# Optimization experiments

Hardware: AMD Instinct MI355X
Metric: run time of the kernel (lower is better)

Reference implementation:

```python
import jax, jax.numpy as jnp
import numpy as np

MARGIN = 1.0


def setup_inputs() -> dict:
    key = jax.random.key(0)
    k1, k2, k3 = jax.random.split(key, 3)
    B, D, C = 16384, 256, 2000
    pred_embedding = jax.random.normal(k1, (B, D), dtype=jnp.float32)
    batch_label = jax.random.randint(k2, (B,), 0, C, dtype=jnp.int64)
    train_classes = jnp.arange(C, dtype=jnp.int64)
    train_sig = jax.random.normal(k3, (D, C), dtype=jnp.float32)
    return {
        "pred_embedding": pred_embedding,
        "batch_label": batch_label,
        "train_classes": train_classes,
        "train_sig": train_sig,
    }


def reference(pred_embedding, batch_label, train_classes, train_sig):
    # scores[j, k] = <pred_embedding[j], train_sig[:, train_classes[k]]>
    # Single GEMM replaces the per-pair dot-product loops.
    sig_cols = train_sig[:, train_classes]            # [D, C]
    scores = jnp.einsum("bd,dc->bc", pred_embedding, sig_cols)  # [B, C]
    # ground-truth class score per row: <XW_j, train_sig[:, y_j]>
    gt = jnp.einsum("bd,db->b", pred_embedding, train_sig[:, batch_label])  # [B]
    # exclude the class equal to the row label
    mask = (train_classes[None, :] != batch_label[:, None])  # [B, C] bool
    hinge = jnp.maximum(MARGIN + scores - gt[:, None], 0.0)
    loss = jnp.sum(jnp.where(mask, hinge, 0.0))
    return loss
```

## Files before the change

### kernel.cpp

```cpp
#include <hip/hip_runtime.h>

#define B_SZ 16384
#define D_SZ 256
#define C_SZ 2000
#define C_PAD 2048
#define MARGIN_F 1.0f
#define NBLK 1024

typedef __bf16 bf16x8 __attribute__((ext_vector_type(8)));
typedef float floatx16 __attribute__((ext_vector_type(16)));

__device__ inline void gld_lds16(const void* g, void* l) {
  __builtin_amdgcn_global_load_lds(
      (const __attribute__((address_space(1))) void*)g,
      (__attribute__((address_space(3))) void*)l, 16, 0, 0);
}


__global__ __launch_bounds__(256) void prep_kernel(
    const float* __restrict__ pred, const float* __restrict__ sig,
    const int* __restrict__ label, __bf16* __restrict__ predf,
    __bf16* __restrict__ sigf, float* __restrict__ gt,
    float* __restrict__ corr) {
  int bid = (int)blockIdx.x;
  int tid = threadIdx.x;
  if (bid < 512) {
    __shared__ float ldsP[32][257];
#pragma unroll
    for (int it = 0; it < 8; it++) {
      int idx = it * 1024 + tid * 4;
      int r = idx >> 8, c = idx & 255;
      float4 v = *(const float4*)(pred + (size_t)(bid * 32 + r) * D_SZ + c);
      ldsP[r][c] = v.x; ldsP[r][c + 1] = v.y;
      ldsP[r][c + 2] = v.z; ldsP[r][c + 3] = v.w;
    }
    __syncthreads();
#pragma unroll
    for (int it = 0; it < 4; it++) {
      int ch = it * 256 + tid;
      int lane = ch & 63, ks = ch >> 6;
      int r = lane & 31, kb = ks * 16 + (lane >> 5) * 8;
      bf16x8 o;
#pragma unroll
      for (int j = 0; j < 8; j++) o[j] = (__bf16)ldsP[r][kb + j];
      *(bf16x8*)(predf + ((size_t)(bid * 16 + ks) * 64 + lane) * 8) = o;
    }
    int lane = tid & 63, w = tid >> 6;
    for (int rr = 0; rr < 8; rr++) {
      int r = w * 8 + rr;
      int row = bid * 32 + r;
      int lbl = label[row];
      float sf = 0.f, sb = 0.f;
#pragma unroll
      for (int i = 0; i < 4; i++) {
        float p = ldsP[r][lane * 4 + i];
        float s = sig[(size_t)(lane * 4 + i) * C_SZ + lbl];
        sf += p * s;
        sb += (float)(__bf16)p * (float)(__bf16)s;
      }
#pragma unroll
      for (int off = 32; off > 0; off >>= 1) {
        sf += __shfl_down(sf, off, 64);
        sb += __shfl_down(sb, off, 64);
      }
      if (lane == 0) {
        gt[row] = sf;
        corr[row] = fmaxf(MARGIN_F + sb - sf, 0.f);
      }
    }
  } else {
    int ct = bid - 512;
#pragma unroll
    for (int it = 0; it < 4; it++) {
      int ch = it * 256 + tid;
      int lane = ch & 63, ks = ch >> 6;
      int col = ct * 32 + (lane & 31);
      int kb = ks * 16 + (lane >> 5) * 8;
      bf16x8 o;
      if (col < C_SZ) {
#pragma unroll
        for (int j = 0; j < 8; j++) o[j] = (__bf16)sig[(size_t)(kb + j) * C_SZ + col];
      } else {
#pragma unroll
        for (int j = 0; j < 8; j++) o[j] = (__bf16)0.f;
      }
      *(bf16x8*)(sigf + ((size_t)(ct * 16 + ks) * 64 + lane) * 8) = o;
    }
  }
}

__global__ __launch_bounds__(256, 2) void mfma_fused_kernel(
    const __bf16* __restrict__ predf, const __bf16* __restrict__ sigf,
    const float* __restrict__ gt, float* __restrict__ partial) {
  __shared__ __bf16 Bs[4096 * 8];
  __shared__ float red[4];
  int tid = threadIdx.x;
  int lane = tid & 63;
  int w = tid >> 6;
  int kh = lane >> 5, lm = lane & 31;
  int bid = (int)blockIdx.x;
  int i = bid >> 3;
  int rsb = (bid & 7) * 8 + (i & 7);
  int cg = i >> 3;

#pragma unroll
  for (int s = 0; s < 16; s++) {
    int q0 = s * 256 + w * 64;
    gld_lds16(sigf + ((size_t)cg * 4096 + q0 + lane) * 8, (void*)(Bs + (size_t)q0 * 8));
  }

  bf16x8 afr[2][16];
#pragma unroll
  for (int rt = 0; rt < 2; rt++)
#pragma unroll
    for (int ks = 0; ks < 16; ks++)
      afr[rt][ks] = *(const bf16x8*)(predf +
          (((size_t)(rsb * 8 + w * 2 + rt) * 16 + ks) * 64 + lane) * 8);

  float mgv[2][16];
#pragma unroll
  for (int rt = 0; rt < 2; rt++)
#pragma unroll
    for (int reg = 0; reg < 16; reg++) {
      int row = rsb * 256 + w * 64 + rt * 32 + (reg & 3) + 8 * (reg >> 2) + 4 * kh;
      mgv[rt][reg] = MARGIN_F - gt[row];
    }
  __syncthreads();

  float sum = 0.f;
  for (int ct = 0; ct < 4; ct++) {
    floatx16 acc0 = {}, acc1 = {};
#pragma unroll
    for (int ks = 0; ks < 16; ks++) {
      bf16x8 bfr = *(const bf16x8*)(Bs + (size_t)((ct * 16 + ks) * 64 + lane) * 8);
      acc0 = __builtin_amdgcn_mfma_f32_32x32x16_bf16(afr[0][ks], bfr, acc0, 0, 0, 0);
      acc1 = __builtin_amdgcn_mfma_f32_32x32x16_bf16(afr[1][ks], bfr, acc1, 0, 0, 0);
    }
    int col = cg * 128 + ct * 32 + lm;
    float keep = (col < C_SZ) ? 1.f : 0.f;
#pragma unroll
    for (int reg = 0; reg < 16; reg++) {
      sum += keep * fmaxf(acc0[reg] + mgv[0][reg], 0.f);
      sum += keep * fmaxf(acc1[reg] + mgv[1][reg], 0.f);
    }
  }
#pragma unroll
  for (int off = 32; off > 0; off >>= 1) sum += __shfl_down(sum, off, 64);
  if (lane == 0) red[w] = sum;
  __syncthreads();
  if (tid == 0) partial[bid] = red[0] + red[1] + red[2] + red[3];
}

__global__ __launch_bounds__(256) void reduce_kernel(
    const float* __restrict__ partial, const float* __restrict__ corr,
    float* __restrict__ out) {
  int tid = threadIdx.x;
  float s = 0.f;
  for (int i = tid; i < NBLK; i += 256) s += partial[i];
  for (int i = tid * 4; i < B_SZ; i += 1024) {
    float4 c = *(const float4*)(corr + i);
    s -= c.x + c.y + c.z + c.w;
  }
#pragma unroll
  for (int off = 32; off > 0; off >>= 1) s += __shfl_down(s, off, 64);
  __shared__ float red[4];
  if ((tid & 63) == 0) red[tid >> 6] = s;
  __syncthreads();
  if (tid == 0) out[0] = red[0] + red[1] + red[2] + red[3];
}

extern "C" void kernel_launch(void* const* d_in, const int* in_sizes, int n_in,
                              void* d_out, int out_size, void* d_ws, size_t ws_size,
                              hipStream_t stream) {
  const float* pred  = (const float*)d_in[0];
  const int*   label = (const int*)d_in[1];
  const float* sig   = (const float*)d_in[3];
  float* out = (float*)d_out;

  float*  gt      = (float*)d_ws;
  float*  corr    = (float*)((char*)d_ws + (64 << 10));
  float*  partial = (float*)((char*)d_ws + (128 << 10));
  __bf16* predf   = (__bf16*)((char*)d_ws + (192 << 10));
  __bf16* sigf    = (__bf16*)((char*)d_ws + (192 << 10) + (8 << 20));

  prep_kernel<<<576, 256, 0, stream>>>(pred, sig, label, predf, sigf, gt, corr);
  mfma_fused_kernel<<<NBLK, 256, 0, stream>>>(predf, sigf, gt, partial);
  reduce_kernel<<<1, 256, 0, stream>>>(partial, corr, out);
}
```

Before: 111.7 us.

## Split sig conversion, compute gt in bf16, fold final reduce into GEMM kernel

Moves the sig-to-bf16 packing into its own small kernel so prep can read the label column from the packed bf16 buffer. The ground-truth score is now computed in bf16 so it matches the GEMM diagonal, which removes the correction array. The separate reduce kernel is replaced by a last-block-done atomic counter inside the MFMA kernel, which subtracts the constant B*margin for the label column. This trades one launch for another, still three kernels in total. It also adds a serial dependency between the sig and prep stages and an atomic/fence tail in the main kernel.

```diff
diff --git a/kernel.cpp b/kernel.cpp
--- a/kernel.cpp
+++ b/kernel.cpp
@@ -8,6 +8,7 @@
 #define NBLK 1024
 
 typedef __bf16 bf16x8 __attribute__((ext_vector_type(8)));
+typedef __bf16 bf16x4 __attribute__((ext_vector_type(4)));
 typedef float floatx16 __attribute__((ext_vector_type(16)));
 
 __device__ inline void gld_lds16(const void* g, void* l) {
@@ -17,83 +18,84 @@
 }
 
 
+__global__ __launch_bounds__(256) void sigf_kernel(
+    const float* __restrict__ sig, __bf16* __restrict__ sigf,
+    unsigned int* __restrict__ cnt) {
+  if (blockIdx.x == 0 && threadIdx.x == 0) *cnt = 0u;
+  int ct = (int)blockIdx.x;
+#pragma unroll
+  for (int it = 0; it < 4; it++) {
+    int ch = it * 256 + threadIdx.x;
+    int lane = ch & 63, ks = ch >> 6;
+    int col = ct * 32 + (lane & 31);
+    int kb = ks * 16 + (lane >> 5) * 8;
+    bf16x8 o;
+    if (col < C_SZ) {
+#pragma unroll
+      for (int j = 0; j < 8; j++) o[j] = (__bf16)sig[(size_t)(kb + j) * C_SZ + col];
+    } else {
+#pragma unroll
+      for (int j = 0; j < 8; j++) o[j] = (__bf16)0.f;
+    }
+    *(bf16x8*)(sigf + ((size_t)(ct * 16 + ks) * 64 + lane) * 8) = o;
+  }
+}
+
 __global__ __launch_bounds__(256) void prep_kernel(
-    const float* __restrict__ pred, const float* __restrict__ sig,
+    const float* __restrict__ pred, const __bf16* __restrict__ sigf,
     const int* __restrict__ label, __bf16* __restrict__ predf,
-    __bf16* __restrict__ sigf, float* __restrict__ gt,
-    float* __restrict__ corr) {
+    float* __restrict__ gt) {
+  __shared__ float ldsP[32][257];
   int bid = (int)blockIdx.x;
   int tid = threadIdx.x;
-  if (bid < 512) {
-    __shared__ float ldsP[32][257];
 #pragma unroll
-    for (int it = 0; it < 8; it++) {
-      int idx = it * 1024 + tid * 4;
-      int r = idx >> 8, c = idx & 255;
-      float4 v = *(const float4*)(pred + (size_t)(bid * 32 + r) * D_SZ + c);
-      ldsP[r][c] = v.x; ldsP[r][c + 1] = v.y;
-      ldsP[r][c + 2] = v.z; ldsP[r][c + 3] = v.w;
-    }
-    __syncthreads();
+  for (int it = 0; it < 8; it++) {
+    int idx = it * 1024 + tid * 4;
+    int r = idx >> 8, c = idx & 255;
+    float4 v = *(const float4*)(pred + (size_t)(bid * 32 + r) * D_SZ + c);
+    ldsP[r][c] = v.x; ldsP[r][c + 1] = v.y;
+    ldsP[r][c + 2] = v.z; ldsP[r][c + 3] = v.w;
+  }
+  __syncthreads();
 #pragma unroll
-    for (int it = 0; it < 4; it++) {
-      int ch = it * 256 + tid;
-      int lane = ch & 63, ks = ch >> 6;
-      int r = lane & 31, kb = ks * 16 + (lane >> 5) * 8;
-      bf16x8 o;
+  for (int it = 0; it < 4; it++) {
+    int ch = it * 256 + tid;
+    int lane = ch & 63, ks = ch >> 6;
+    int r = lane & 31, kb = ks * 16 + (lane >> 5) * 8;
+    bf16x8 o;
 #pragma unroll
-      for (int j = 0; j < 8; j++) o[j] = (__bf16)ldsP[r][kb + j];
-      *(bf16x8*)(predf + ((size_t)(bid * 16 + ks) * 64 + lane) * 8) = o;
-    }
-    int lane = tid & 63, w = tid >> 6;
-    for (int rr = 0; rr < 8; rr++) {
-      int r = w * 8 + rr;
-      int row = bid * 32 + r;
-      int lbl = label[row];
-      float sf = 0.f, sb = 0.f;
+    for (int j = 0; j < 8; j++) o[j] = (__bf16)ldsP[r][kb + j];
+    *(bf16x8*)(predf + ((size_t)(bid * 16 + ks) * 64 + lane) * 8) = o;
+  }
+  int lane = tid & 63, w = tid >> 6;
+  for (int rr = 0; rr < 8; rr++) {
+    int r = w * 8 + rr;
+    int row = bid * 32 + r;
+    int lbl = label[row];
+    int tile = lbl >> 5, l5 = lbl & 31;
+    int k0 = lane * 4;
+    int ks = k0 >> 4;
+    int kh = (k0 >> 3) & 1;
+    int j0 = k0 & 7;
+    bf16x4 sb = *(const bf16x4*)(sigf +
+        (((size_t)(tile * 16 + ks) * 64) + kh * 32 + l5) * 8 + j0);
+    float s = 0.f;
 #pragma unroll
-      for (int i = 0; i < 4; i++) {
-        float p = ldsP[r][lane * 4 + i];
-        float s = sig[(size_t)(lane * 4 + i) * C_SZ + lbl];
-        sf += p * s;
-        sb += (float)(__bf16)p * (float)(__bf16)s;
-      }
+    for (int i = 0; i < 4; i++)
+      s += (float)(__bf16)ldsP[r][k0 + i] * (float)sb[i];
 #pragma unroll
-      for (int off = 32; off > 0; off >>= 1) {
-        sf += __shfl_down(sf, off, 64);
-        sb += __shfl_down(sb, off, 64);
-      }
-      if (lane == 0) {
-        gt[row] = sf;
-        corr[row] = fmaxf(MARGIN_F + sb - sf, 0.f);
-      }
-    }
-  } else {
-    int ct = bid - 512;
-#pragma unroll
-    for (int it = 0; it < 4; it++) {
-      int ch = it * 256 + tid;
-      int lane = ch & 63, ks = ch >> 6;
-      int col = ct * 32 + (lane & 31);
-      int kb = ks * 16 + (lane >> 5) * 8;
-      bf16x8 o;
-      if (col < C_SZ) {
-#pragma unroll
-        for (int j = 0; j < 8; j++) o[j] = (__bf16)sig[(size_t)(kb + j) * C_SZ + col];
-      } else {
-#pragma unroll
-        for (int j = 0; j < 8; j++) o[j] = (__bf16)0.f;
-      }
-      *(bf16x8*)(sigf + ((size_t)(ct * 16 + ks) * 64 + lane) * 8) = o;
-    }
+    for (int off = 32; off > 0; off >>= 1) s += __shfl_down(s, off, 64);
+    if (lane == 0) gt[row] = s;
   }
 }
 
 __global__ __launch_bounds__(256, 2) void mfma_fused_kernel(
     const __bf16* __restrict__ predf, const __bf16* __restrict__ sigf,
-    const float* __restrict__ gt, float* __restrict__ partial) {
+    const float* __restrict__ gt, float* __restrict__ partial,
+    unsigned int* __restrict__ cnt, float* __restrict__ out) {
   __shared__ __bf16 Bs[4096 * 8];
   __shared__ float red[4];
+  __shared__ float lastFlag;
   int tid = threadIdx.x;
   int lane = tid & 63;
   int w = tid >> 6;
@@ -148,25 +150,23 @@
   for (int off = 32; off > 0; off >>= 1) sum += __shfl_down(sum, off, 64);
   if (lane == 0) red[w] = sum;
   __syncthreads();
-  if (tid == 0) partial[bid] = red[0] + red[1] + red[2] + red[3];
-}
-
-__global__ __launch_bounds__(256) void reduce_kernel(
-    const float* __restrict__ partial, const float* __restrict__ corr,
-    float* __restrict__ out) {
-  int tid = threadIdx.x;
-  float s = 0.f;
-  for (int i = tid; i < NBLK; i += 256) s += partial[i];
-  for (int i = tid * 4; i < B_SZ; i += 1024) {
-    float4 c = *(const float4*)(corr + i);
-    s -= c.x + c.y + c.z + c.w;
+  if (tid == 0) {
+    partial[bid] = red[0] + red[1] + red[2] + red[3];
+    __threadfence();
+    unsigned int old = atomicAdd(cnt, 1u);
+    lastFlag = (old == NBLK - 1) ? 1.f : 0.f;
   }
+  __syncthreads();
+  if (lastFlag != 0.f) {
+    float s = (tid == 0) ? -(float)B_SZ * MARGIN_F : 0.f;
+    for (int p = tid; p < NBLK; p += 256)
+      s += atomicAdd(&partial[p], 0.f);
 #pragma unroll
-  for (int off = 32; off > 0; off >>= 1) s += __shfl_down(s, off, 64);
-  __shared__ float red[4];
-  if ((tid & 63) == 0) red[tid >> 6] = s;
-  __syncthreads();
-  if (tid == 0) out[0] = red[0] + red[1] + red[2] + red[3];
+    for (int off = 32; off > 0; off >>= 1) s += __shfl_down(s, off, 64);
+    if (lane == 0) red[w] = s;
+    __syncthreads();
+    if (tid == 0) out[0] = red[0] + red[1] + red[2] + red[3];
+  }
 }
 
 extern "C" void kernel_launch(void* const* d_in, const int* in_sizes, int n_in,
@@ -177,13 +177,13 @@
   const float* sig   = (const float*)d_in[3];
   float* out = (float*)d_out;
 
-  float*  gt      = (float*)d_ws;
-  float*  corr    = (float*)((char*)d_ws + (64 << 10));
-  float*  partial = (float*)((char*)d_ws + (128 << 10));
-  __bf16* predf   = (__bf16*)((char*)d_ws + (192 << 10));
-  __bf16* sigf    = (__bf16*)((char*)d_ws + (192 << 10) + (8 << 20));
+  float*        gt      = (float*)d_ws;
+  float*        partial = (float*)((char*)d_ws + (64 << 10));
+  unsigned int* cnt     = (unsigned int*)((char*)d_ws + (68 << 10));
+  __bf16*       predf   = (__bf16*)((char*)d_ws + (128 << 10));
+  __bf16*       sigf    = (__bf16*)((char*)d_ws + (128 << 10) + (8 << 20));
 
-  prep_kernel<<<576, 256, 0, stream>>>(pred, sig, label, predf, sigf, gt, corr);
-  mfma_fused_kernel<<<NBLK, 256, 0, stream>>>(predf, sigf, gt, partial);
-  reduce_kernel<<<1, 256, 0, stream>>>(partial, corr, out);
+  sigf_kernel<<<64, 256, 0, stream>>>(sig, sigf, cnt);
+  prep_kernel<<<512, 256, 0, stream>>>(pred, sigf, label, predf, gt);
+  mfma_fused_kernel<<<NBLK, 256, 0, stream>>>(predf, sigf, gt, partial, cnt, out);
 }
```

After: 114.2 us. 1.02x slower.

## Switch GEMM operands from bf16 to fp8 MFMA and drop diagonal correction pass

Applied to the files above, without the earlier changes.

Quantizes the prediction and signature matrices to fp8 instead of bf16 and uses the fp8 32x32x16 MFMA. This halves operand bytes and LDS footprint and doubles matrix throughput. The ground-truth score is now computed from fp8-rounded values, so the diagonal hinge term equals exactly the margin and is subtracted as a constant instead of through a per-row correction array. The cost is much lower precision in the loss sum, and the result now depends on fp8 rounding matching between the GEMM and the scalar path.

```diff
diff --git a/kernel.cpp b/kernel.cpp
--- a/kernel.cpp
+++ b/kernel.cpp
@@ -7,7 +7,6 @@
 #define MARGIN_F 1.0f
 #define NBLK 1024
 
-typedef __bf16 bf16x8 __attribute__((ext_vector_type(8)));
 typedef float floatx16 __attribute__((ext_vector_type(16)));
 
 __device__ inline void gld_lds16(const void* g, void* l) {
@@ -17,22 +16,31 @@
 }
 
 
+__device__ inline int2 pack8_fp8(const float* v) {
+  int lo = __builtin_amdgcn_cvt_pk_fp8_f32(v[0], v[1], 0, false);
+  lo = __builtin_amdgcn_cvt_pk_fp8_f32(v[2], v[3], lo, true);
+  int hi = __builtin_amdgcn_cvt_pk_fp8_f32(v[4], v[5], 0, false);
+  hi = __builtin_amdgcn_cvt_pk_fp8_f32(v[6], v[7], hi, true);
+  return make_int2(lo, hi);
+}
+__device__ inline float rt_fp8(float x) {
+  int p = __builtin_amdgcn_cvt_pk_fp8_f32(x, x, 0, false);
+  return __builtin_amdgcn_cvt_f32_fp8(p, 0);
+}
+
 __global__ __launch_bounds__(256) void prep_kernel(
     const float* __restrict__ pred, const float* __restrict__ sig,
-    const int* __restrict__ label, __bf16* __restrict__ predf,
-    __bf16* __restrict__ sigf, float* __restrict__ gt,
-    float* __restrict__ corr) {
+    const int* __restrict__ label, char* __restrict__ predq,
+    char* __restrict__ sigq, float* __restrict__ gt) {
   int bid = (int)blockIdx.x;
   int tid = threadIdx.x;
   if (bid < 512) {
-    __shared__ float ldsP[32][257];
+    __shared__ float ldsP[32][260];
 #pragma unroll
     for (int it = 0; it < 8; it++) {
       int idx = it * 1024 + tid * 4;
       int r = idx >> 8, c = idx & 255;
-      float4 v = *(const float4*)(pred + (size_t)(bid * 32 + r) * D_SZ + c);
-      ldsP[r][c] = v.x; ldsP[r][c + 1] = v.y;
-      ldsP[r][c + 2] = v.z; ldsP[r][c + 3] = v.w;
+      *(float4*)&ldsP[r][c] = *(const float4*)(pred + (size_t)(bid * 32 + r) * D_SZ + c);
     }
     __syncthreads();
 #pragma unroll
@@ -40,33 +48,24 @@
       int ch = it * 256 + tid;
       int lane = ch & 63, ks = ch >> 6;
       int r = lane & 31, kb = ks * 16 + (lane >> 5) * 8;
-      bf16x8 o;
+      float v[8];
 #pragma unroll
-      for (int j = 0; j < 8; j++) o[j] = (__bf16)ldsP[r][kb + j];
-      *(bf16x8*)(predf + ((size_t)(bid * 16 + ks) * 64 + lane) * 8) = o;
+      for (int j = 0; j < 8; j++) v[j] = ldsP[r][kb + j];
+      *(int2*)(predq + ((size_t)(bid * 16 + ks) * 64 + lane) * 8) = pack8_fp8(v);
     }
     int lane = tid & 63, w = tid >> 6;
     for (int rr = 0; rr < 8; rr++) {
       int r = w * 8 + rr;
       int row = bid * 32 + r;
       int lbl = label[row];
-      float sf = 0.f, sb = 0.f;
+      float s = 0.f;
 #pragma unroll
-      for (int i = 0; i < 4; i++) {
-        float p = ldsP[r][lane * 4 + i];
-        float s = sig[(size_t)(lane * 4 + i) * C_SZ + lbl];
-        sf += p * s;
-        sb += (float)(__bf16)p * (float)(__bf16)s;
-      }
+      for (int i = 0; i < 4; i++)
+        s += rt_fp8(ldsP[r][lane * 4 + i]) *
+             rt_fp8(sig[(size_t)(lane * 4 + i) * C_SZ + lbl]);
 #pragma unroll
-      for (int off = 32; off > 0; off >>= 1) {
-        sf += __shfl_down(sf, off, 64);
-        sb += __shfl_down(sb, off, 64);
-      }
-      if (lane == 0) {
-        gt[row] = sf;
-        corr[row] = fmaxf(MARGIN_F + sb - sf, 0.f);
-      }
+      for (int off = 32; off > 0; off >>= 1) s += __shfl_down(s, off, 64);
+      if (lane == 0) gt[row] = s;
     }
   } else {
     int ct = bid - 512;
@@ -76,23 +75,19 @@
       int lane = ch & 63, ks = ch >> 6;
       int col = ct * 32 + (lane & 31);
       int kb = ks * 16 + (lane >> 5) * 8;
-      bf16x8 o;
-      if (col < C_SZ) {
+      float v[8];
 #pragma unroll
-        for (int j = 0; j < 8; j++) o[j] = (__bf16)sig[(size_t)(kb + j) * C_SZ + col];
-      } else {
-#pragma unroll
-        for (int j = 0; j < 8; j++) o[j] = (__bf16)0.f;
-      }
-      *(bf16x8*)(sigf + ((size_t)(ct * 16 + ks) * 64 + lane) * 8) = o;
+      for (int j = 0; j < 8; j++)
+        v[j] = (col < C_SZ) ? sig[(size_t)(kb + j) * C_SZ + col] : 0.f;
+      *(int2*)(sigq + ((size_t)(ct * 16 + ks) * 64 + lane) * 8) = pack8_fp8(v);
     }
   }
 }
 
-__global__ __launch_bounds__(256, 2) void mfma_fused_kernel(
-    const __bf16* __restrict__ predf, const __bf16* __restrict__ sigf,
+__global__ __launch_bounds__(256) void mfma_fused_kernel(
+    const char* __restrict__ predq, const char* __restrict__ sigq,
     const float* __restrict__ gt, float* __restrict__ partial) {
-  __shared__ __bf16 Bs[4096 * 8];
+  __shared__ char Bs[4096 * 8];
   __shared__ float red[4];
   int tid = threadIdx.x;
   int lane = tid & 63;
@@ -104,17 +99,17 @@
   int cg = i >> 3;
 
 #pragma unroll
-  for (int s = 0; s < 16; s++) {
+  for (int s = 0; s < 8; s++) {
     int q0 = s * 256 + w * 64;
-    gld_lds16(sigf + ((size_t)cg * 4096 + q0 + lane) * 8, (void*)(Bs + (size_t)q0 * 8));
+    gld_lds16(sigq + ((size_t)cg * 2048 + q0 + lane) * 16, (void*)(Bs + (size_t)q0 * 16));
   }
 
-  bf16x8 afr[2][16];
+  long afr[2][16];
 #pragma unroll
   for (int rt = 0; rt < 2; rt++)
 #pragma unroll
     for (int ks = 0; ks < 16; ks++)
-      afr[rt][ks] = *(const bf16x8*)(predf +
+      afr[rt][ks] = *(const long*)(predq +
           (((size_t)(rsb * 8 + w * 2 + rt) * 16 + ks) * 64 + lane) * 8);
 
   float mgv[2][16];
@@ -128,13 +123,14 @@
   __syncthreads();
 
   float sum = 0.f;
+#pragma unroll
   for (int ct = 0; ct < 4; ct++) {
     floatx16 acc0 = {}, acc1 = {};
 #pragma unroll
     for (int ks = 0; ks < 16; ks++) {
-      bf16x8 bfr = *(const bf16x8*)(Bs + (size_t)((ct * 16 + ks) * 64 + lane) * 8);
-      acc0 = __builtin_amdgcn_mfma_f32_32x32x16_bf16(afr[0][ks], bfr, acc0, 0, 0, 0);
-      acc1 = __builtin_amdgcn_mfma_f32_32x32x16_bf16(afr[1][ks], bfr, acc1, 0, 0, 0);
+      long b = *(const long*)(Bs + (size_t)((ct * 16 + ks) * 64 + lane) * 8);
+      acc0 = __builtin_amdgcn_mfma_f32_32x32x16_fp8_fp8(afr[0][ks], b, acc0, 0, 0, 0);
+      acc1 = __builtin_amdgcn_mfma_f32_32x32x16_fp8_fp8(afr[1][ks], b, acc1, 0, 0, 0);
     }
     int col = cg * 128 + ct * 32 + lm;
     float keep = (col < C_SZ) ? 1.f : 0.f;
@@ -152,21 +148,19 @@
 }
 
 __global__ __launch_bounds__(256) void reduce_kernel(
-    const float* __restrict__ partial, const float* __restrict__ corr,
-    float* __restrict__ out) {
+    const float* __restrict__ partial, float* __restrict__ out) {
   int tid = threadIdx.x;
   float s = 0.f;
-  for (int i = tid; i < NBLK; i += 256) s += partial[i];
-  for (int i = tid * 4; i < B_SZ; i += 1024) {
-    float4 c = *(const float4*)(corr + i);
-    s -= c.x + c.y + c.z + c.w;
+  for (int i = tid * 4; i < NBLK; i += 1024) {
+    float4 p = *(const float4*)(partial + i);
+    s += p.x + p.y + p.z + p.w;
   }
 #pragma unroll
   for (int off = 32; off > 0; off >>= 1) s += __shfl_down(s, off, 64);
   __shared__ float red[4];
   if ((tid & 63) == 0) red[tid >> 6] = s;
   __syncthreads();
-  if (tid == 0) out[0] = red[0] + red[1] + red[2] + red[3];
+  if (tid == 0) out[0] = red[0] + red[1] + red[2] + red[3] - (float)B_SZ * MARGIN_F;
 }
 
 extern "C" void kernel_launch(void* const* d_in, const int* in_sizes, int n_in,
@@ -177,13 +171,12 @@
   const float* sig   = (const float*)d_in[3];
   float* out = (float*)d_out;
 
-  float*  gt      = (float*)d_ws;
-  float*  corr    = (float*)((char*)d_ws + (64 << 10));
-  float*  partial = (float*)((char*)d_ws + (128 << 10));
-  __bf16* predf   = (__bf16*)((char*)d_ws + (192 << 10));
-  __bf16* sigf    = (__bf16*)((char*)d_ws + (192 << 10) + (8 << 20));
+  float* gt      = (float*)d_ws;
+  float* partial = (float*)((char*)d_ws + (64 << 10));
+  char*  predq   = (char*)d_ws + (128 << 10);
+  char*  sigq    = (char*)d_ws + (128 << 10) + (4 << 20);
 
-  prep_kernel<<<576, 256, 0, stream>>>(pred, sig, label, predf, sigf, gt, corr);
-  mfma_fused_kernel<<<NBLK, 256, 0, stream>>>(predf, sigf, gt, partial);
-  reduce_kernel<<<1, 256, 0, stream>>>(partial, corr, out);
+  prep_kernel<<<576, 256, 0, stream>>>(pred, sig, label, predq, sigq, gt);
+  mfma_fused_kernel<<<NBLK, 256, 0, stream>>>(predq, sigq, gt, partial);
+  reduce_kernel<<<1, 256, 0, stream>>>(partial, out);
 }
```

Result: faster. 104.4 us (-6.6%).
